# Kernel tuning notes

Hardware: AMD Instinct MI355X
Metric: run time of the kernel (lower is better)

Reference implementation:

```python
import jax, jax.numpy as jnp
import numpy as np

B, H, NI, NQ = 4096, 1024, 4096, 2048


def setup_inputs() -> dict:
    key = jax.random.key(0)
    ks = jax.random.split(key, 12)
    state = jax.random.normal(ks[0], (B, H), jnp.float32)
    inputX = jax.random.normal(ks[1], (B, NI), jnp.float32)
    # one-hot next-question vector
    q_idx = jax.random.randint(ks[2], (B,), 0, NQ)
    inputY = jax.nn.one_hot(q_idx, NQ, dtype=jnp.float32)
    truth = jax.random.bernoulli(ks[3], 0.5, (B,)).astype(jnp.float32)
    # torch.nn.Linear default init: U(-1/sqrt(fan_in), 1/sqrt(fan_in)), weight (out,in)
    def lin(kw, kb, out_d, in_d):
        bound = 1.0 / np.sqrt(in_d)
        W = jax.random.uniform(kw, (out_d, in_d), jnp.float32, -bound, bound)
        b = jax.random.uniform(kb, (out_d,), jnp.float32, -bound, bound)
        return W, b
    W_t, b_t = lin(ks[4], ks[5], H, H)    # transfer: n_hidden -> n_hidden
    W_x, b_x = lin(ks[6], ks[7], H, NI)   # linear_x: n_input -> n_hidden
    W_y, b_y = lin(ks[8], ks[9], NQ, H)   # linear_y: n_hidden -> n_questions
    return {"state": state, "inputX": inputX, "inputY": inputY, "truth": truth,
            "W_t": W_t, "b_t": b_t, "W_x": W_x, "b_x": b_x, "W_y": W_y, "b_y": b_y}


def reference(state, inputX, inputY, truth, W_t, b_t, W_x, b_x, W_y, b_y):
    # two small linears + tanh -> new hidden state
    linM = state @ W_t.T + b_t                       # (B, H)
    linX = inputX @ W_x.T + b_x                      # (B, H)
    hidden = jnp.tanh(linM + linX)                   # (B, H)
    # prediction head: linear + sigmoid, mask-select via one-hot sum
    pred_output = jax.nn.sigmoid(hidden @ W_y.T + b_y)  # (B, NQ)
    pred = jnp.sum(pred_output * inputY, axis=1)        # (B,)
    # binary cross entropy, sum reduction; torch clamps log terms at -100
    log_p = jnp.maximum(jnp.log(pred), -100.0)
    log_1mp = jnp.maximum(jnp.log1p(-pred), -100.0)
    err = -jnp.sum(truth * log_p + (1.0 - truth) * log_1mp)
    return (pred, err, hidden)
```

## Files before the change

### kernel.cpp

```cpp
#include <hip/hip_runtime.h>
#include <stdint.h>
#include <math.h>

#define B_DIM 4096
#define H_DIM 1024
#define NI_DIM 4096
#define NQ_DIM 2048
#define K_DIM 5120
#define NKT 160

typedef __attribute__((ext_vector_type(8))) short short8;
typedef __attribute__((ext_vector_type(4))) float f32x4;

__device__ __forceinline__ unsigned short f2bf(float f) {
  unsigned u = __float_as_uint(f);
  u += 0x7FFFu + ((u >> 16) & 1u);
  return (unsigned short)(u >> 16);
}
__device__ __forceinline__ float bf2f(unsigned short s) {
  return __uint_as_float(((unsigned)s) << 16);
}
__device__ __forceinline__ unsigned pkbf(float a, float b) {
  unsigned r;
  asm("v_cvt_pk_bf16_f32 %0, %1, %2" : "=v"(r) : "v"(a), "v"(b));
  return r;
}

__device__ __forceinline__ void gload_lds16(const void* g, void* l) {
  __builtin_amdgcn_global_load_lds(
      (__attribute__((address_space(1))) void*)(uintptr_t)g,
      (__attribute__((address_space(3))) void*)l, 16, 0, 0);
}

__global__ __launch_bounds__(256) void cast_v4(
    const float* __restrict__ X0, const float* __restrict__ X1,
    const float* __restrict__ W0, const float* __restrict__ W1,
    short* __restrict__ Xc, short* __restrict__ Wc) {
  __shared__ __align__(16) short lds[16384];
  int bt = blockIdx.x;
  const float *s0, *s1;
  short* dst;
  if (bt < (B_DIM / 128) * (NKT / 4)) { s0 = X0; s1 = X1; dst = Xc; }
  else { bt -= (B_DIM / 128) * (NKT / 4); s0 = W0; s1 = W1; dst = Wc; }
  const int rowTile = bt / (NKT / 4);
  const int K0 = (bt % (NKT / 4)) * 4;
  const float* src;
  int cols, colBase;
  if (K0 < 32) { src = s0; cols = 1024; colBase = K0 * 32; }
  else         { src = s1; cols = 4096; colBase = (K0 - 32) * 32; }
  const int tid = threadIdx.x;
  const int kc = tid & 31;
  const int r0 = tid >> 5;
#pragma unroll
  for (int i = 0; i < 16; ++i) {
    int r = r0 + i * 8;
    float4 v = *(const float4*)(src +
        (long long)(rowTile * 128 + r) * cols + colBase + kc * 4);
    uint2 o;
    o.x = pkbf(v.x, v.y);
    o.y = pkbf(v.z, v.w);
    int l = (kc >> 1) * 128 + r;
    int p = l ^ ((l >> 7) & 7);
    *(uint2*)(&lds[p * 8 + (kc & 1) * 4]) = o;
  }
  __syncthreads();
  short* dbase = dst + ((long long)rowTile * NKT + K0) * 4096;
#pragma unroll
  for (int i = 0; i < 8; ++i) {
    int c = tid + i * 256;
    int p = c ^ ((c >> 7) & 7);
    *(short8*)(dbase + c * 8) = *(const short8*)(&lds[p * 8]);
  }
}

__device__ __forceinline__ int ep_swz(int col, int rw) {
  int byte = col * 256 + rw * 2;
  byte ^= ((col ^ (col >> 3)) & 7) << 4;
  return byte;
}

__global__ __launch_bounds__(256, 4) void gemm_splitk(
    const short* __restrict__ Xc, const short* __restrict__ Wc,
    short* __restrict__ P, int ntk) {
  __shared__ __align__(16) short SH[16384];
  const int tid = threadIdx.x;
  const int lane = tid & 63;
  const int wid = tid >> 6;
  const int wm = wid >> 1, wn = wid & 1;
  const int fr = lane & 15, fq = lane >> 4;

  const int nwg = gridDim.x;
  const int orig = blockIdx.x;
  const int cpx = nwg >> 3;
  const int swz = (orig & 7) * cpx + (orig >> 3);
  const int bz = swz >> 8;
  const int bm = (swz >> 3) & 31;
  const int bn = swz & 7;
  const int kt0 = bz * ntk;

  const int c0 = tid, c1 = tid + 256;
  const short* gA = Xc + (((long long)bm * NKT + kt0) << 12);
  const short* gB = Wc + (((long long)bn * NKT + kt0) << 12);

  f32x4 acc[4][4] = {};

  gload_lds16(gA + c0 * 8, &SH[c0 * 8]);
  gload_lds16(gA + c1 * 8, &SH[c1 * 8]);
  gload_lds16(gB + c0 * 8, &SH[8192 + c0 * 8]);
  gload_lds16(gB + c1 * 8, &SH[8192 + c1 * 8]);
  __syncthreads();

  int cur = 0;
  for (int t = 0; t < ntk; ++t) {
    if (t + 1 < ntk) {
      const short* nA = gA + (long long)(t + 1) * 4096;
      const short* nB = gB + (long long)(t + 1) * 4096;
      short* lA = &SH[(cur ^ 1) * 4096];
      short* lB = &SH[8192 + (cur ^ 1) * 4096];
      gload_lds16(nA + c0 * 8, lA + c0 * 8);
      gload_lds16(nA + c1 * 8, lA + c1 * 8);
      gload_lds16(nB + c0 * 8, lB + c0 * 8);
      gload_lds16(nB + c1 * 8, lB + c1 * 8);
    }
    const short* a_base = &SH[cur * 4096];
    const short* b_base = &SH[8192 + cur * 4096];
    short8 av[4], bv[4];
#pragma unroll
    for (int i = 0; i < 4; i++) {
      av[i] = *(const short8*)(a_base + (fq * 128 + wm * 64 + i * 16 + fr) * 8);
      bv[i] = *(const short8*)(b_base + (fq * 128 + wn * 64 + i * 16 + fr) * 8);
    }
#pragma unroll
    for (int mi = 0; mi < 4; mi++)
#pragma unroll
      for (int ni = 0; ni < 4; ni++)
        acc[mi][ni] = __builtin_amdgcn_mfma_f32_16x16x32_bf16(
            av[mi], bv[ni], acc[mi][ni], 0, 0, 0);
    __syncthreads();
    cur ^= 1;
  }

#pragma unroll
  for (int ni = 0; ni < 4; ni++) {
    int col = wn * 64 + ni * 16 + fr;
#pragma unroll
    for (int mi = 0; mi < 4; mi++) {
      int rw = wm * 64 + mi * 16 + fq * 4;
      unsigned lo = (unsigned)f2bf(acc[mi][ni][0]) |
                    ((unsigned)f2bf(acc[mi][ni][1]) << 16);
      unsigned hi = (unsigned)f2bf(acc[mi][ni][2]) |
                    ((unsigned)f2bf(acc[mi][ni][3]) << 16);
      uint2 pk; pk.x = lo; pk.y = hi;
      *(uint2*)((char*)SH + ep_swz(col, rw)) = pk;
    }
  }
  __syncthreads();
  short* Pp = P + (long long)bz * B_DIM * H_DIM;
#pragma unroll
  for (int h = 0; h < 8; ++h) {
    int chunk = tid + h * 256;
    int rr = chunk >> 4;
    int j = chunk & 15;
    short8 o;
#pragma unroll
    for (int k = 0; k < 8; ++k) {
      o[k] = *(const short*)((char*)SH + ep_swz(j * 8 + k, rr));
    }
    *(short8*)(Pp + (long long)(bm * 128 + rr) * H_DIM + bn * 128 + j * 8) = o;
  }
}

__global__ __launch_bounds__(256) void fuse_row(
    const short* __restrict__ P, const float* __restrict__ bt,
    const float* __restrict__ bx, const float* __restrict__ Y,
    const float* __restrict__ truth, const float* __restrict__ Wy,
    const float* __restrict__ by, float* __restrict__ predOut,
    float* __restrict__ hidden, float* __restrict__ bce, int S) {
  const int b = blockIdx.x;
  const int tid = threadIdx.x;
  __shared__ int s_cnt;
  __shared__ int s_idx[8];
  __shared__ float s_val[8];
  __shared__ float s_red[4];
  if (tid == 0) s_cnt = 0;

  const int c = tid * 4;
  float s0 = 0.f, s1 = 0.f, s2 = 0.f, s3 = 0.f;
  for (int z = 0; z < S; ++z) {
    const short* Pr = P + ((long long)z * B_DIM + b) * H_DIM + c;
    uint2 u = *(const uint2*)Pr;
    s0 += bf2f((unsigned short)(u.x & 0xffff));
    s1 += bf2f((unsigned short)(u.x >> 16));
    s2 += bf2f((unsigned short)(u.y & 0xffff));
    s3 += bf2f((unsigned short)(u.y >> 16));
  }
  float4 bt4 = *(const float4*)(bt + c);
  float4 bx4 = *(const float4*)(bx + c);
  float h0 = tanhf(s0 + bt4.x + bx4.x);
  float h1 = tanhf(s1 + bt4.y + bx4.y);
  float h2 = tanhf(s2 + bt4.z + bx4.z);
  float h3 = tanhf(s3 + bt4.w + bx4.w);
  float* Hr = hidden + (long long)b * H_DIM + c;
  Hr[0] = h0; Hr[1] = h1; Hr[2] = h2; Hr[3] = h3;

  __syncthreads();
  const float4* Yr = (const float4*)(Y + (long long)b * NQ_DIM);
#pragma unroll
  for (int hh = 0; hh < NQ_DIM / 4 / 256; ++hh) {
    int j = tid + hh * 256;
    float4 v = Yr[j];
    if (v.x != 0.0f) { int p = atomicAdd(&s_cnt, 1); if (p < 8) { s_idx[p] = 4 * j;     s_val[p] = v.x; } }
    if (v.y != 0.0f) { int p = atomicAdd(&s_cnt, 1); if (p < 8) { s_idx[p] = 4 * j + 1; s_val[p] = v.y; } }
    if (v.z != 0.0f) { int p = atomicAdd(&s_cnt, 1); if (p < 8) { s_idx[p] = 4 * j + 2; s_val[p] = v.z; } }
    if (v.w != 0.0f) { int p = atomicAdd(&s_cnt, 1); if (p < 8) { s_idx[p] = 4 * j + 3; s_val[p] = v.w; } }
  }
  __syncthreads();
  int cnt = s_cnt < 8 ? s_cnt : 8;
  float predv = 0.0f;
  for (int it = 0; it < cnt; ++it) {
    int q = s_idx[it];
    float4 w = *(const float4*)(Wy + (long long)q * H_DIM + c);
    float part = h0 * w.x + h1 * w.y + h2 * w.z + h3 * w.w;
#pragma unroll
    for (int off = 32; off > 0; off >>= 1) part += __shfl_down(part, off, 64);
    if ((tid & 63) == 0) s_red[tid >> 6] = part;
    __syncthreads();
    if (tid == 0) {
      float z = s_red[0] + s_red[1] + s_red[2] + s_red[3] + by[q];
      float p = 1.0f / (1.0f + expf(-z));
      predv += s_val[it] * p;
    }
    __syncthreads();
  }
  if (tid == 0) {
    predOut[b] = predv;
    float t = truth[b];
    float lp = fmaxf(logf(predv), -100.0f);
    float l1p = fmaxf(log1pf(-predv), -100.0f);
    bce[b] = -(t * lp + (1.0f - t) * l1p);
  }
}

__global__ __launch_bounds__(256) void reduce_err(
    const float* __restrict__ bce, float* __restrict__ errOut) {
  float s = 0.0f;
  for (int i = threadIdx.x; i < B_DIM; i += 256) s += bce[i];
#pragma unroll
  for (int off = 32; off > 0; off >>= 1) s += __shfl_down(s, off, 64);
  __shared__ float red[4];
  if ((threadIdx.x & 63) == 0) red[threadIdx.x >> 6] = s;
  __syncthreads();
  if (threadIdx.x == 0) errOut[0] = red[0] + red[1] + red[2] + red[3];
}

extern "C" void kernel_launch(void* const* d_in, const int* in_sizes, int n_in,
                              void* d_out, int out_size, void* d_ws, size_t ws_size,
                              hipStream_t stream) {
  (void)in_sizes; (void)n_in; (void)out_size;
  const float* state  = (const float*)d_in[0];
  const float* inputX = (const float*)d_in[1];
  const float* inputY = (const float*)d_in[2];
  const float* truth  = (const float*)d_in[3];
  const float* W_t    = (const float*)d_in[4];
  const float* b_t    = (const float*)d_in[5];
  const float* W_x    = (const float*)d_in[6];
  const float* b_x    = (const float*)d_in[7];
  const float* W_y    = (const float*)d_in[8];
  const float* b_y    = (const float*)d_in[9];

  const size_t XC_B = (size_t)B_DIM * K_DIM * 2;
  const size_t WC_B = (size_t)H_DIM * K_DIM * 2;
  const size_t PART = (size_t)B_DIM * H_DIM * 2;

  int S = 1;
  if (ws_size >= XC_B + WC_B + 4 * PART + 16384) S = 4;
  else if (ws_size >= XC_B + WC_B + 2 * PART + 16384) S = 2;

  short* Xc = (short*)d_ws;
  short* Wc = (short*)((char*)d_ws + XC_B);
  short* P  = (short*)((char*)d_ws + XC_B + WC_B);
  float* bce = (float*)((char*)d_ws + XC_B + WC_B + (size_t)S * PART);

  float* predOut = (float*)d_out;
  float* errOut  = predOut + B_DIM;
  float* hidden  = predOut + B_DIM + 1;

  cast_v4<<<(B_DIM / 128 + H_DIM / 128) * (NKT / 4), 256, 0, stream>>>(
      state, inputX, W_t, W_x, Xc, Wc);

  gemm_splitk<<<256 * S, 256, 0, stream>>>(Xc, Wc, P, NKT / S);

  fuse_row<<<B_DIM, 256, 0, stream>>>(P, b_t, b_x, inputY, truth, W_y, b_y,
                                      predOut, hidden, bce, S);
  reduce_err<<<1, 256, 0, stream>>>(bce, errOut);
}
```

Baseline: 94.22 us.

## Enlarge GEMM block tile to 256x256 with 512 threads and deeper K steps

Replaces the 128x128 split-K GEMM with a 256x256 output tile per workgroup, using 8 waves that each compute 128x64, and loads two K sub-tiles per iteration into a 128KB double-buffered LDS. This raises arithmetic intensity and cuts global and LDS traffic per MFMA, and halves the number of barriers per K unit. In exchange the grid drops to 64*S workgroups, which may underfill the 256 CUs. The large LDS footprint and register use also limit occupancy, and the epilogue swizzle is widened to match.

```diff
diff --git a/kernel.cpp b/kernel.cpp
--- a/kernel.cpp
+++ b/kernel.cpp
@@ -74,99 +74,117 @@
 }
 
 __device__ __forceinline__ int ep_swz(int col, int rw) {
-  int byte = col * 256 + rw * 2;
+  int byte = col * 512 + rw * 2;
   byte ^= ((col ^ (col >> 3)) & 7) << 4;
   return byte;
 }
 
-__global__ __launch_bounds__(256, 4) void gemm_splitk(
+__global__ __launch_bounds__(512, 2) void gemm_256(
     const short* __restrict__ Xc, const short* __restrict__ Wc,
-    short* __restrict__ P, int ntk) {
-  __shared__ __align__(16) short SH[16384];
+    short* __restrict__ P, int ntile) {
+  __shared__ __align__(16) short SH[65536];
   const int tid = threadIdx.x;
   const int lane = tid & 63;
   const int wid = tid >> 6;
-  const int wm = wid >> 1, wn = wid & 1;
+  const int wr = wid >> 2, wc = wid & 3;
   const int fr = lane & 15, fq = lane >> 4;
 
   const int nwg = gridDim.x;
   const int orig = blockIdx.x;
   const int cpx = nwg >> 3;
   const int swz = (orig & 7) * cpx + (orig >> 3);
-  const int bz = swz >> 8;
-  const int bm = (swz >> 3) & 31;
-  const int bn = swz & 7;
-  const int kt0 = bz * ntk;
-
-  const int c0 = tid, c1 = tid + 256;
-  const short* gA = Xc + (((long long)bm * NKT + kt0) << 12);
-  const short* gB = Wc + (((long long)bn * NKT + kt0) << 12);
-
-  f32x4 acc[4][4] = {};
-
-  gload_lds16(gA + c0 * 8, &SH[c0 * 8]);
-  gload_lds16(gA + c1 * 8, &SH[c1 * 8]);
-  gload_lds16(gB + c0 * 8, &SH[8192 + c0 * 8]);
-  gload_lds16(gB + c1 * 8, &SH[8192 + c1 * 8]);
+  const int bz = swz >> 6;
+  const int bm = (swz >> 2) & 15;
+  const int bn = swz & 3;
+  const int kt0 = bz * (2 * ntile);
+
+  const short* gA0 = Xc + ((long long)((bm * 2 + 0) * NKT + kt0) << 12);
+  const short* gA2 = Xc + ((long long)((bm * 2 + 1) * NKT + kt0) << 12);
+  const short* gB0 = Wc + ((long long)((bn * 2 + 0) * NKT + kt0) << 12);
+  const short* gB2 = Wc + ((long long)((bn * 2 + 1) * NKT + kt0) << 12);
+
+  f32x4 acc[8][4] = {};
+
+  const int t8 = tid * 8;
+
+  {
+    gload_lds16(gA0 + t8, &SH[t8]);
+    gload_lds16(gA0 + 4096 + t8, &SH[4096 + t8]);
+    gload_lds16(gA2 + t8, &SH[8192 + t8]);
+    gload_lds16(gA2 + 4096 + t8, &SH[12288 + t8]);
+    gload_lds16(gB0 + t8, &SH[16384 + t8]);
+    gload_lds16(gB0 + 4096 + t8, &SH[20480 + t8]);
+    gload_lds16(gB2 + t8, &SH[24576 + t8]);
+    gload_lds16(gB2 + 4096 + t8, &SH[28672 + t8]);
+  }
   __syncthreads();
 
   int cur = 0;
-  for (int t = 0; t < ntk; ++t) {
-    if (t + 1 < ntk) {
-      const short* nA = gA + (long long)(t + 1) * 4096;
-      const short* nB = gB + (long long)(t + 1) * 4096;
-      short* lA = &SH[(cur ^ 1) * 4096];
-      short* lB = &SH[8192 + (cur ^ 1) * 4096];
-      gload_lds16(nA + c0 * 8, lA + c0 * 8);
-      gload_lds16(nA + c1 * 8, lA + c1 * 8);
-      gload_lds16(nB + c0 * 8, lB + c0 * 8);
-      gload_lds16(nB + c1 * 8, lB + c1 * 8);
-    }
-    const short* a_base = &SH[cur * 4096];
-    const short* b_base = &SH[8192 + cur * 4096];
-    short8 av[4], bv[4];
-#pragma unroll
-    for (int i = 0; i < 4; i++) {
-      av[i] = *(const short8*)(a_base + (fq * 128 + wm * 64 + i * 16 + fr) * 8);
-      bv[i] = *(const short8*)(b_base + (fq * 128 + wn * 64 + i * 16 + fr) * 8);
-    }
-#pragma unroll
-    for (int mi = 0; mi < 4; mi++)
-#pragma unroll
-      for (int ni = 0; ni < 4; ni++)
-        acc[mi][ni] = __builtin_amdgcn_mfma_f32_16x16x32_bf16(
-            av[mi], bv[ni], acc[mi][ni], 0, 0, 0);
+  for (int t = 0; t < ntile; ++t) {
+    if (t + 1 < ntile) {
+      long long off = (long long)(t + 1) * 8192 + t8;
+      short* L = &SH[(cur ^ 1) * 32768];
+      gload_lds16(gA0 + off, L + t8);
+      gload_lds16(gA0 + 4096 + off, L + 4096 + t8);
+      gload_lds16(gA2 + off, L + 8192 + t8);
+      gload_lds16(gA2 + 4096 + off, L + 12288 + t8);
+      gload_lds16(gB0 + off, L + 16384 + t8);
+      gload_lds16(gB0 + 4096 + off, L + 20480 + t8);
+      gload_lds16(gB2 + off, L + 24576 + t8);
+      gload_lds16(gB2 + 4096 + off, L + 28672 + t8);
+    }
+    const short* aS = &SH[cur * 32768] + wr * 8192;
+    const short* bS = &SH[cur * 32768 + 16384] + (wc >> 1) * 8192;
+    const int brow = (wc & 1) * 64;
+#pragma unroll
+    for (int ks = 0; ks < 2; ++ks) {
+      short8 av[8], bv[4];
+#pragma unroll
+      for (int mi = 0; mi < 8; ++mi)
+        av[mi] = *(const short8*)(aS + ks * 4096 +
+                                  (fq * 128 + mi * 16 + fr) * 8);
+#pragma unroll
+      for (int ni = 0; ni < 4; ++ni)
+        bv[ni] = *(const short8*)(bS + ks * 4096 +
+                                  (fq * 128 + brow + ni * 16 + fr) * 8);
+#pragma unroll
+      for (int mi = 0; mi < 8; ++mi)
+#pragma unroll
+        for (int ni = 0; ni < 4; ++ni)
+          acc[mi][ni] = __builtin_amdgcn_mfma_f32_16x16x32_bf16(
+              av[mi], bv[ni], acc[mi][ni], 0, 0, 0);
+    }
     __syncthreads();
     cur ^= 1;
   }
 
 #pragma unroll
-  for (int ni = 0; ni < 4; ni++) {
-    int col = wn * 64 + ni * 16 + fr;
-#pragma unroll
-    for (int mi = 0; mi < 4; mi++) {
-      int rw = wm * 64 + mi * 16 + fq * 4;
-      unsigned lo = (unsigned)f2bf(acc[mi][ni][0]) |
-                    ((unsigned)f2bf(acc[mi][ni][1]) << 16);
-      unsigned hi = (unsigned)f2bf(acc[mi][ni][2]) |
-                    ((unsigned)f2bf(acc[mi][ni][3]) << 16);
-      uint2 pk; pk.x = lo; pk.y = hi;
+  for (int ni = 0; ni < 4; ++ni) {
+    int col = wc * 64 + ni * 16 + fr;
+#pragma unroll
+    for (int mi = 0; mi < 8; ++mi) {
+      int rw = wr * 128 + mi * 16 + fq * 4;
+      uint2 pk;
+      pk.x = (unsigned)f2bf(acc[mi][ni][0]) |
+             ((unsigned)f2bf(acc[mi][ni][1]) << 16);
+      pk.y = (unsigned)f2bf(acc[mi][ni][2]) |
+             ((unsigned)f2bf(acc[mi][ni][3]) << 16);
       *(uint2*)((char*)SH + ep_swz(col, rw)) = pk;
     }
   }
   __syncthreads();
   short* Pp = P + (long long)bz * B_DIM * H_DIM;
 #pragma unroll
-  for (int h = 0; h < 8; ++h) {
-    int chunk = tid + h * 256;
-    int rr = chunk >> 4;
-    int j = chunk & 15;
+  for (int h = 0; h < 16; ++h) {
+    int chunk = tid + h * 512;
+    int rr = chunk >> 5;
+    int j = chunk & 31;
     short8 o;
 #pragma unroll
     for (int k = 0; k < 8; ++k) {
       o[k] = *(const short*)((char*)SH + ep_swz(j * 8 + k, rr));
     }
-    *(short8*)(Pp + (long long)(bm * 128 + rr) * H_DIM + bn * 128 + j * 8) = o;
+    *(short8*)(Pp + (long long)(bm * 256 + rr) * H_DIM + bn * 256 + j * 8) = o;
   }
 }
 
@@ -288,7 +306,7 @@
   cast_v4<<<(B_DIM / 128 + H_DIM / 128) * (NKT / 4), 256, 0, stream>>>(
       state, inputX, W_t, W_x, Xc, Wc);
 
-  gemm_splitk<<<256 * S, 256, 0, stream>>>(Xc, Wc, P, NKT / S);
+  gemm_256<<<64 * S, 512, 0, stream>>>(Xc, Wc, P, 80 / S);
 
   fuse_row<<<B_DIM, 256, 0, stream>>>(P, b_t, b_x, inputY, truth, W_y, b_y,
                                       predOut, hidden, bce, S);
```

New measurement: 92.51 us, median of 2. Within noise of the previous version (-1.8%).
